# Kernel optimization log

Hardware: AMD Instinct MI355X
Metric: run time of the kernel (lower is better)

The kernel has to match this reference:

```python
import jax, jax.numpy as jnp
import numpy as np

ITEMNUM = 50000
NUM_HEADS = 4
EPS = 1e-8


def _ln(x, g, b):
    m = x.mean(-1, keepdims=True)
    v = ((x - m) ** 2).mean(-1, keepdims=True)
    return (x - m) * jax.lax.rsqrt(v + EPS) * g + b


def _forward(seqs_data, position, seqs, time_emb, pos_table, gate_W, gate_b,
             ln_attn_g, ln_attn_b, qW, qb, kW, kb, vW, vb,
             ln_ffn_g, ln_ffn_b, c1W, c1b, c2W, c2b, last_g, last_b):
    B, L, H = seqs.shape
    nb = qW.shape[0]
    hd = H // NUM_HEADS

    pe = pos_table[position]                      # [B,L,H]
    seqs = seqs + pe
    time = time_emb + pe
    # per-position per-block time gates, [B,L,nb]
    gates = jax.nn.sigmoid(jnp.einsum('blh,nh->bln', time, gate_W) + gate_b)

    keep = (seqs_data != ITEMNUM - 1)[..., None].astype(seqs.dtype)  # [B,L,1]
    seqs = seqs * keep
    tril = jnp.tril(jnp.ones((L, L), dtype=bool))  # causal: keep lower triangle
    neg_inf = jnp.asarray(-jnp.inf, seqs.dtype)
    scale = 1.0 / np.sqrt(hd).astype(np.float32)

    for i in range(nb):
        Q = _ln(seqs, ln_attn_g[i], ln_attn_b[i])
        q = Q @ qW[i].T + qb[i]
        k = time @ kW[i].T + kb[i]
        v = (seqs + time) @ vW[i].T + vb[i]
        # [B,nh,L,hd]
        q = q.reshape(B, L, NUM_HEADS, hd).transpose(0, 2, 1, 3)
        k = k.reshape(B, L, NUM_HEADS, hd).transpose(0, 2, 1, 3)
        v = v.reshape(B, L, NUM_HEADS, hd).transpose(0, 2, 1, 3)
        scores = jnp.einsum('bhqd,bhkd->bhqk', q, k) * scale  # [B,nh,L,L]
        tg = gates[:, :, i]                                   # [B,L]
        gate_mat = tg[:, None, :, None] * tg[:, None, None, :]  # [B,1,L,L] outer product
        scores = jnp.where(tril[None, None], scores * gate_mat, neg_inf)
        attn = jax.nn.softmax(scores, axis=-1)
        out = jnp.einsum('bhqk,bhkd->bhqd', attn, v)
        out = out.transpose(0, 2, 1, 3).reshape(B, L, H)
        x = Q + out
        x = _ln(x, ln_ffn_g[i], ln_ffn_b[i])
        # PointWiseFeedForward: two 1x1 convs == two linears, relu, residual
        h = jax.nn.relu(x @ c1W[i].T + c1b[i])
        seqs = (h @ c2W[i].T + c2b[i] + x) * keep

    return _ln(seqs, last_g, last_b)


def setup_inputs() -> dict:
    key = jax.random.key(0)
    B, L, H, NB, ML = 64, 512, 256, 2, 512
    ks = iter(jax.random.split(key, 32))
    nrm = lambda shape, s=0.05: jax.random.normal(next(ks), shape, jnp.float32) * s
    pos_table = nrm((ML, H), 0.02).at[0].set(0.0)  # padding_idx=0
    inp = {
        'seqs_data': jax.random.randint(next(ks), (B, L), 0, ITEMNUM - 1, jnp.int32),
        'seqs': nrm((B, L, H), 1.0),
        'position': jax.random.randint(next(ks), (B, L), 0, ML, jnp.int32),
        'time_emb': nrm((B, L, H), 1.0),
        'pos_table': pos_table,
        'gate_W': nrm((NB, H)), 'gate_b': jnp.zeros((NB,), jnp.float32),
        'ln_attn_g': jnp.ones((NB, H), jnp.float32), 'ln_attn_b': jnp.zeros((NB, H), jnp.float32),
        'qW': nrm((NB, H, H)), 'qb': jnp.zeros((NB, H), jnp.float32),
        'kW': nrm((NB, H, H)), 'kb': jnp.zeros((NB, H), jnp.float32),
        'vW': nrm((NB, H, H)), 'vb': jnp.zeros((NB, H), jnp.float32),
        'ln_ffn_g': jnp.ones((NB, H), jnp.float32), 'ln_ffn_b': jnp.zeros((NB, H), jnp.float32),
        'c1W': nrm((NB, H, H)), 'c1b': jnp.zeros((NB, H), jnp.float32),
        'c2W': nrm((NB, H, H)), 'c2b': jnp.zeros((NB, H), jnp.float32),
        'last_g': jnp.ones((H,), jnp.float32), 'last_b': jnp.zeros((H,), jnp.float32),
    }
    return inp


def reference(seqs_data, seqs, position, time_emb, pos_table, gate_W, gate_b,
              ln_attn_g, ln_attn_b, qW, qb, kW, kb, vW, vb,
              ln_ffn_g, ln_ffn_b, c1W, c1b, c2W, c2b, last_g, last_b):
    return _forward(seqs_data, position, seqs, time_emb, pos_table, gate_W, gate_b,
                    ln_attn_g, ln_attn_b, qW, qb, kW, kb, vW, vb,
                    ln_ffn_g, ln_ffn_b, c1W, c1b, c2W, c2b, last_g, last_b)
```

## Files before the change

### kernel.cpp

```cpp
#include <hip/hip_runtime.h>
#include <hip/hip_bf16.h>
#include <math.h>

#define NTOK 32768
#define Hdim 256
#define Ldim 512
#define Bdim 64
#define NHEAD 4
#define HD 64
#define PADV 49999

typedef __bf16 bf16x8 __attribute__((ext_vector_type(8)));
typedef float  f32x4  __attribute__((ext_vector_type(4)));

__device__ __forceinline__ unsigned short f2bf(float f) {
    unsigned int u = __float_as_uint(f);
    unsigned int r = (u + 0x7fffu + ((u >> 16) & 1u)) >> 16;
    return (unsigned short)r;
}
__device__ __forceinline__ float bf2f(unsigned short u) {
    return __uint_as_float(((unsigned int)u) << 16);
}

__device__ __forceinline__ void gload16(const void* g, void* l) {
    __builtin_amdgcn_global_load_lds((const __attribute__((address_space(1))) unsigned int*)g,
                                     (__attribute__((address_space(3))) unsigned int*)l,
                                     16, 0, 0);
}

__global__ __launch_bounds__(256)
void castw_kernel(const float* __restrict__ q, const float* __restrict__ k,
                  const float* __restrict__ v, const float* __restrict__ c1,
                  const float* __restrict__ c2, unsigned short* __restrict__ dst) {
    const float* srcs[5] = {q, k, v, c1, c2};
    const float* s = srcs[blockIdx.y];
    int idx = blockIdx.x * 1024 + threadIdx.x * 4;
    float4 f = *(const float4*)(s + idx);
    unsigned short* d = dst + (size_t)blockIdx.y * 131072 + idx;
    d[0] = f2bf(f.x); d[1] = f2bf(f.y); d[2] = f2bf(f.z); d[3] = f2bf(f.w);
}

__global__ __launch_bounds__(256)
void prep_ln_kernel(const int* __restrict__ seqs_data, const float* __restrict__ seqs,
                    const int* __restrict__ position, const float* __restrict__ time_emb,
                    const float* __restrict__ pos_table, const float* __restrict__ gate_W,
                    const float* __restrict__ gate_b,
                    const float* __restrict__ lnG, const float* __restrict__ lnB,
                    unsigned short* __restrict__ Tbf,
                    unsigned short* __restrict__ QXbf,
                    unsigned short* __restrict__ VINbf,
                    float* __restrict__ gates, float* __restrict__ keepv) {
    int tok  = blockIdx.x * 4 + (threadIdx.x >> 6);
    int lane = threadIdx.x & 63;
    size_t off = (size_t)tok * Hdim + lane * 4;
    int pos = position[tok];
    float4 pe = *(const float4*)(pos_table + (size_t)pos * Hdim + lane * 4);
    float4 sq = *(const float4*)(seqs + off);
    float4 tm = *(const float4*)(time_emb + off);
    float keep = (seqs_data[tok] != PADV) ? 1.0f : 0.0f;
    float4 t = {tm.x + pe.x, tm.y + pe.y, tm.z + pe.z, tm.w + pe.w};
    float4 s = {(sq.x + pe.x) * keep, (sq.y + pe.y) * keep,
                (sq.z + pe.z) * keep, (sq.w + pe.w) * keep};
    ushort4 tb = {f2bf(t.x), f2bf(t.y), f2bf(t.z), f2bf(t.w)};
    *(ushort4*)(Tbf + off) = tb;
    float4 gw0 = *(const float4*)(gate_W + lane * 4);
    float4 gw1 = *(const float4*)(gate_W + Hdim + lane * 4);
    float r0 = s.x + s.y + s.z + s.w;
    float r1 = s.x * s.x + s.y * s.y + s.z * s.z + s.w * s.w;
    float r2 = t.x * gw0.x + t.y * gw0.y + t.z * gw0.z + t.w * gw0.w;
    float r3 = t.x * gw1.x + t.y * gw1.y + t.z * gw1.z + t.w * gw1.w;
#pragma unroll
    for (int o = 1; o < 64; o <<= 1) {
        r0 += __shfl_xor(r0, o, 64);
        r1 += __shfl_xor(r1, o, 64);
        r2 += __shfl_xor(r2, o, 64);
        r3 += __shfl_xor(r3, o, 64);
    }
    float mean = r0 * (1.0f / Hdim);
    float var  = fmaxf(r1 * (1.0f / Hdim) - mean * mean, 0.0f);
    float rstd = rsqrtf(var + 1e-8f);
    if (lane == 0) {
        gates[(size_t)tok * 2 + 0] = 1.0f / (1.0f + __expf(-(r2 + gate_b[0])));
        gates[(size_t)tok * 2 + 1] = 1.0f / (1.0f + __expf(-(r3 + gate_b[1])));
        keepv[tok] = keep;
    }
    float4 g4 = *(const float4*)(lnG + lane * 4);
    float4 b4 = *(const float4*)(lnB + lane * 4);
    float4 y = {(s.x - mean) * rstd * g4.x + b4.x, (s.y - mean) * rstd * g4.y + b4.y,
                (s.z - mean) * rstd * g4.z + b4.z, (s.w - mean) * rstd * g4.w + b4.w};
    ushort4 yb = {f2bf(y.x), f2bf(y.y), f2bf(y.z), f2bf(y.w)};
    *(ushort4*)(QXbf + off) = yb;
    ushort4 vb = {f2bf(s.x + t.x), f2bf(s.y + t.y), f2bf(s.z + t.z), f2bf(s.w + t.w)};
    *(ushort4*)(VINbf + off) = vb;
}

__global__ __launch_bounds__(256)
void ln2_kernel(unsigned short* QXbf, const unsigned short* __restrict__ QA,
                const float* __restrict__ lnG, const float* __restrict__ lnB) {
    int tok  = blockIdx.x * 4 + (threadIdx.x >> 6);
    int lane = threadIdx.x & 63;
    size_t off = (size_t)tok * Hdim + lane * 4;
    ushort4 q = *(const ushort4*)(QXbf + off);
    ushort4 a = *(const ushort4*)(QA + off);
    float4 x = {bf2f(q.x) + bf2f(a.x), bf2f(q.y) + bf2f(a.y),
                bf2f(q.z) + bf2f(a.z), bf2f(q.w) + bf2f(a.w)};
    float r0 = x.x + x.y + x.z + x.w;
    float r1 = x.x * x.x + x.y * x.y + x.z * x.z + x.w * x.w;
#pragma unroll
    for (int o = 1; o < 64; o <<= 1) {
        r0 += __shfl_xor(r0, o, 64);
        r1 += __shfl_xor(r1, o, 64);
    }
    float mean = r0 * (1.0f / Hdim);
    float var  = fmaxf(r1 * (1.0f / Hdim) - mean * mean, 0.0f);
    float rstd = rsqrtf(var + 1e-8f);
    float4 g4 = *(const float4*)(lnG + lane * 4);
    float4 b4 = *(const float4*)(lnB + lane * 4);
    ushort4 yb = {f2bf((x.x - mean) * rstd * g4.x + b4.x),
                  f2bf((x.y - mean) * rstd * g4.y + b4.y),
                  f2bf((x.z - mean) * rstd * g4.z + b4.z),
                  f2bf((x.w - mean) * rstd * g4.w + b4.w)};
    *(ushort4*)(QXbf + off) = yb;
}

__global__ __launch_bounds__(256)
void lnout_kernel(const unsigned short* __restrict__ Zbf,
                  unsigned short* QXbf,
                  const unsigned short* __restrict__ Tbf,
                  const float* __restrict__ keepv,
                  const float* __restrict__ lnG, const float* __restrict__ lnB,
                  float* __restrict__ outF,
                  unsigned short* __restrict__ outVIN) {
    int tok  = blockIdx.x * 4 + (threadIdx.x >> 6);
    int lane = threadIdx.x & 63;
    size_t off = (size_t)tok * Hdim + lane * 4;
    ushort4 z = *(const ushort4*)(Zbf + off);
    ushort4 x = *(const ushort4*)(QXbf + off);
    float kf = keepv[tok];
    float4 s = {(bf2f(z.x) + bf2f(x.x)) * kf, (bf2f(z.y) + bf2f(x.y)) * kf,
                (bf2f(z.z) + bf2f(x.z)) * kf, (bf2f(z.w) + bf2f(x.w)) * kf};
    float r0 = s.x + s.y + s.z + s.w;
    float r1 = s.x * s.x + s.y * s.y + s.z * s.z + s.w * s.w;
#pragma unroll
    for (int o = 1; o < 64; o <<= 1) {
        r0 += __shfl_xor(r0, o, 64);
        r1 += __shfl_xor(r1, o, 64);
    }
    float mean = r0 * (1.0f / Hdim);
    float var  = fmaxf(r1 * (1.0f / Hdim) - mean * mean, 0.0f);
    float rstd = rsqrtf(var + 1e-8f);
    float4 g4 = *(const float4*)(lnG + lane * 4);
    float4 b4 = *(const float4*)(lnB + lane * 4);
    float4 y = {(s.x - mean) * rstd * g4.x + b4.x, (s.y - mean) * rstd * g4.y + b4.y,
                (s.z - mean) * rstd * g4.z + b4.z, (s.w - mean) * rstd * g4.w + b4.w};
    if (outF) {
        *(float4*)(outF + off) = y;
    } else {
        ushort4 yb = {f2bf(y.x), f2bf(y.y), f2bf(y.z), f2bf(y.w)};
        *(ushort4*)(QXbf + off) = yb;
        ushort4 t = *(const ushort4*)(Tbf + off);
        ushort4 vb = {f2bf(s.x + bf2f(t.x)), f2bf(s.y + bf2f(t.y)),
                      f2bf(s.z + bf2f(t.z)), f2bf(s.w + bf2f(t.w))};
        *(ushort4*)(outVIN + off) = vb;
    }
}

#define GBM 128
#define GBN 128
#define GBK 32

__global__ __launch_bounds__(256)
void gemm_qkv_kernel(const unsigned short* __restrict__ QXbf,
                     const unsigned short* __restrict__ Tbf,
                     const unsigned short* __restrict__ VINbf,
                     const unsigned short* __restrict__ qW,
                     const unsigned short* __restrict__ kW,
                     const unsigned short* __restrict__ vW,
                     const float* __restrict__ qb, const float* __restrict__ kb,
                     const float* __restrict__ vb,
                     unsigned short* __restrict__ Qbf,
                     unsigned short* __restrict__ Kbf,
                     unsigned short* __restrict__ VT) {
    __shared__ __align__(16) char smem[128 * 136 * 2];
    __bf16 (*As)[GBK] = (__bf16 (*)[GBK])smem;
    __bf16 (*Ws)[GBK] = (__bf16 (*)[GBK])(smem + 8192);
    __bf16 (*Ct)[136] = (__bf16 (*)[136])smem;
    int z = blockIdx.z;
    const unsigned short* A = (z == 0) ? QXbf : (z == 1) ? Tbf : VINbf;
    const unsigned short* W = (z == 0) ? qW : (z == 1) ? kW : vW;
    const float* bias       = (z == 0) ? qb : (z == 1) ? kb : vb;

    int tid = threadIdx.x, lane = tid & 63, w = tid >> 6;
    int wr = w >> 1, wc = w & 1;
    int m0 = blockIdx.y * GBM, n0 = blockIdx.x * GBN;
    f32x4 acc[4][4];
#pragma unroll
    for (int i = 0; i < 4; ++i)
#pragma unroll
        for (int j = 0; j < 4; ++j) acc[i][j] = (f32x4)(0.0f);
    int cA = tid, cB = tid + 256;
    int rA = cA >> 2, kA = (cA & 3) * 8;
    int rB = cB >> 2, kB = (cB & 3) * 8;
    int colq = lane & 15, kq = (lane >> 4) * 8;
    for (int kc = 0; kc < Hdim; kc += GBK) {
        __syncthreads();
        gload16(A + (size_t)(m0 + rA) * Hdim + kc + kA, (__bf16*)As + cA * 8);
        gload16(A + (size_t)(m0 + rB) * Hdim + kc + kB, (__bf16*)As + cB * 8);
        gload16(W + (size_t)(n0 + rA) * Hdim + kc + kA, (__bf16*)Ws + cA * 8);
        gload16(W + (size_t)(n0 + rB) * Hdim + kc + kB, (__bf16*)Ws + cB * 8);
        __syncthreads();
        bf16x8 af[4], bfr[4];
#pragma unroll
        for (int i = 0; i < 4; ++i)
            af[i] = *(const bf16x8*)&As[wr * 64 + i * 16 + colq][kq];
#pragma unroll
        for (int j = 0; j < 4; ++j)
            bfr[j] = *(const bf16x8*)&Ws[wc * 64 + j * 16 + colq][kq];
#pragma unroll
        for (int i = 0; i < 4; ++i)
#pragma unroll
            for (int j = 0; j < 4; ++j)
                acc[i][j] = __builtin_amdgcn_mfma_f32_16x16x32_bf16(af[i], bfr[j], acc[i][j], 0, 0, 0);
    }
    int rowq = (lane >> 4) * 4;
    if (z < 2) {
        unsigned short* outBF = (z == 0) ? Qbf : Kbf;
#pragma unroll
        for (int i = 0; i < 4; ++i)
#pragma unroll
            for (int r = 0; r < 4; ++r) {
                int m = m0 + wr * 64 + i * 16 + rowq + r;
#pragma unroll
                for (int j = 0; j < 4; ++j) {
                    int n = n0 + wc * 64 + j * 16 + colq;
                    outBF[(size_t)m * Hdim + n] = f2bf(acc[i][j][r] + bias[n]);
                }
            }
    } else {
        __syncthreads();
#pragma unroll
        for (int i = 0; i < 4; ++i)
#pragma unroll
            for (int r = 0; r < 4; ++r) {
                int ml = wr * 64 + i * 16 + rowq + r;
#pragma unroll
                for (int j = 0; j < 4; ++j) {
                    int nl = wc * 64 + j * 16 + colq;
                    Ct[nl][ml] = (__bf16)(acc[i][j][r] + bias[n0 + nl]);
                }
            }
        __syncthreads();
        int bb = m0 >> 9, l0 = m0 & 511;
#pragma unroll
        for (int it = 0; it < 8; ++it) {
            int c = tid + it * 256;
            int nl = c >> 4;
            int o8 = (c & 15) * 8;
            int n = n0 + nl;
            int hh = n >> 6, dd = n & 63;
            bf16x8 v = *(const bf16x8*)&Ct[nl][o8];
            *(bf16x8*)(VT + ((((size_t)bb * NHEAD + hh) * HD + dd) * Ldim + l0 + o8)) = v;
        }
    }
}

__global__ __launch_bounds__(256)
void gemm_plain_kernel(const unsigned short* __restrict__ A,
                       const unsigned short* __restrict__ W,
                       const float* __restrict__ bias,
                       unsigned short* __restrict__ outBF, int doRelu) {
    __shared__ __bf16 As[GBM][GBK];
    __shared__ __bf16 Ws[GBN][GBK];
    int tid = threadIdx.x, lane = tid & 63, w = tid >> 6;
    int wr = w >> 1, wc = w & 1;
    int m0 = blockIdx.y * GBM, n0 = blockIdx.x * GBN;
    f32x4 acc[4][4];
#pragma unroll
    for (int i = 0; i < 4; ++i)
#pragma unroll
        for (int j = 0; j < 4; ++j) acc[i][j] = (f32x4)(0.0f);
    int cA = tid, cB = tid + 256;
    int rA = cA >> 2, kA = (cA & 3) * 8;
    int rB = cB >> 2, kB = (cB & 3) * 8;
    int colq = lane & 15, kq = (lane >> 4) * 8;
    for (int kc = 0; kc < Hdim; kc += GBK) {
        __syncthreads();
        gload16(A + (size_t)(m0 + rA) * Hdim + kc + kA, (__bf16*)As + cA * 8);
        gload16(A + (size_t)(m0 + rB) * Hdim + kc + kB, (__bf16*)As + cB * 8);
        gload16(W + (size_t)(n0 + rA) * Hdim + kc + kA, (__bf16*)Ws + cA * 8);
        gload16(W + (size_t)(n0 + rB) * Hdim + kc + kB, (__bf16*)Ws + cB * 8);
        __syncthreads();
        bf16x8 af[4], bfr[4];
#pragma unroll
        for (int i = 0; i < 4; ++i)
            af[i] = *(const bf16x8*)&As[wr * 64 + i * 16 + colq][kq];
#pragma unroll
        for (int j = 0; j < 4; ++j)
            bfr[j] = *(const bf16x8*)&Ws[wc * 64 + j * 16 + colq][kq];
#pragma unroll
        for (int i = 0; i < 4; ++i)
#pragma unroll
            for (int j = 0; j < 4; ++j)
                acc[i][j] = __builtin_amdgcn_mfma_f32_16x16x32_bf16(af[i], bfr[j], acc[i][j], 0, 0, 0);
    }
    int rowq = (lane >> 4) * 4;
#pragma unroll
    for (int i = 0; i < 4; ++i)
#pragma unroll
        for (int r = 0; r < 4; ++r) {
            int m = m0 + wr * 64 + i * 16 + rowq + r;
#pragma unroll
            for (int j = 0; j < 4; ++j) {
                int n = n0 + wc * 64 + j * 16 + colq;
                float v = acc[i][j][r] + bias[n];
                if (doRelu) v = fmaxf(v, 0.0f);
                outBF[(size_t)m * Hdim + n] = f2bf(v);
            }
        }
}

#define AK_STRIDE 72
#define AV_STRIDE 520
#define ATTN_LDS (512 * AK_STRIDE * 2 + 64 * AV_STRIDE * 2 + 128 * AK_STRIDE * 2)
__global__ __launch_bounds__(512, 1)
void attn_mfma_kernel(const unsigned short* __restrict__ Qg,
                      const unsigned short* __restrict__ Kg,
                      const unsigned short* __restrict__ VTg,
                      const float* __restrict__ gates,
                      unsigned short* __restrict__ Ob, int blk) {
    extern __shared__ __align__(16) char smem[];
    __bf16 (*Ks)[AK_STRIDE]  = (__bf16 (*)[AK_STRIDE])smem;
    __bf16 (*VTs)[AV_STRIDE] = (__bf16 (*)[AV_STRIDE])(smem + 512 * AK_STRIDE * 2);
    __bf16 (*QPs)[AK_STRIDE] = (__bf16 (*)[AK_STRIDE])(smem + 512 * AK_STRIDE * 2 + 64 * AV_STRIDE * 2);
    int h = blockIdx.x & 3, b = blockIdx.x >> 2;
    int tid = threadIdx.x, lane = tid & 63, w = tid >> 6;
    int colq = lane & 15, grp = lane >> 4;
    int rowq = grp * 4, kq = grp * 8;

    size_t baseK = (size_t)b * Ldim * Hdim + h * HD;
#pragma unroll
    for (int it = 0; it < 8; ++it) {
        int c = tid + it * 512;
        int r = c >> 3, o = (c & 7) * 8;
        *(bf16x8*)&Ks[r][o] = *(const bf16x8*)(Kg + baseK + (size_t)r * Hdim + o);
    }
    size_t baseV = ((size_t)b * NHEAD + h) * HD * Ldim;
#pragma unroll
    for (int it = 0; it < 8; ++it) {
        int c = tid + it * 512;
        int d = c >> 6, k = (c & 63) * 8;
        *(bf16x8*)&VTs[d][k] = *(const bf16x8*)(VTg + baseV + (size_t)d * Ldim + k);
    }

    const float lscale = 0.125f * 1.44269504f;
    for (int qt = 0; qt < 4; ++qt) {
        int q0 = qt * 128;
        __syncthreads();
#pragma unroll
        for (int it = 0; it < 2; ++it) {
            int c = tid + it * 512;
            int r = c >> 3, o = (c & 7) * 8;
            *(bf16x8*)&QPs[r][o] =
                *(const bf16x8*)(Qg + (size_t)(b * Ldim + q0 + r) * Hdim + h * HD + o);
        }
        float gql[4];
#pragma unroll
        for (int r = 0; r < 4; ++r)
            gql[r] = gates[((size_t)b * Ldim + q0 + w * 16 + rowq + r) * 2 + blk] * lscale;
        __syncthreads();
        bf16x8 afq0 = *(const bf16x8*)&QPs[w * 16 + colq][kq];
        bf16x8 afq1 = *(const bf16x8*)&QPs[w * 16 + colq][32 + kq];

        float lrun[4] = {0.0f, 0.0f, 0.0f, 0.0f};
        f32x4 accO[4];
#pragma unroll
        for (int jd = 0; jd < 4; ++jd) accO[jd] = (f32x4)(0.0f);

        int nkt = 2 * qt + 2;
        for (int kt = 0; kt < nkt; ++kt) {
            int k0 = kt * 64;
            f32x4 s[4];
#pragma unroll
            for (int j = 0; j < 4; ++j) s[j] = (f32x4)(0.0f);
#pragma unroll
            for (int j = 0; j < 4; ++j) {
                bf16x8 bk0 = *(const bf16x8*)&Ks[k0 + j * 16 + colq][kq];
                bf16x8 bk1 = *(const bf16x8*)&Ks[k0 + j * 16 + colq][32 + kq];
                s[j] = __builtin_amdgcn_mfma_f32_16x16x32_bf16(afq0, bk0, s[j], 0, 0, 0);
                s[j] = __builtin_amdgcn_mfma_f32_16x16x32_bf16(afq1, bk1, s[j], 0, 0, 0);
            }
            float gkv[4];
#pragma unroll
            for (int j = 0; j < 4; ++j)
                gkv[j] = gates[((size_t)b * Ldim + k0 + j * 16 + colq) * 2 + blk];
#pragma unroll
            for (int r = 0; r < 4; ++r) {
                int qg = q0 + w * 16 + rowq + r;
                float su = 0.0f;
                float p[4];
#pragma unroll
                for (int j = 0; j < 4; ++j) {
                    int kg = k0 + j * 16 + colq;
                    float v = s[j][r] * gql[r] * gkv[j];
                    v = (kg > qg) ? -1e38f : v;
                    float e = exp2f(v);
                    p[j] = e;
                    su += e;
                }
#pragma unroll
                for (int off = 1; off < 16; off <<= 1)
                    su += __shfl_xor(su, off, 16);
                lrun[r] += su;
#pragma unroll
                for (int j = 0; j < 4; ++j)
                    QPs[w * 16 + rowq + r][j * 16 + colq] = (__bf16)p[j];
            }
            bf16x8 ap0 = *(const bf16x8*)&QPs[w * 16 + colq][kq];
            bf16x8 ap1 = *(const bf16x8*)&QPs[w * 16 + colq][32 + kq];
#pragma unroll
            for (int jd = 0; jd < 4; ++jd) {
                bf16x8 bv0 = *(const bf16x8*)&VTs[jd * 16 + colq][k0 + kq];
                bf16x8 bv1 = *(const bf16x8*)&VTs[jd * 16 + colq][k0 + 32 + kq];
                accO[jd] = __builtin_amdgcn_mfma_f32_16x16x32_bf16(ap0, bv0, accO[jd], 0, 0, 0);
                accO[jd] = __builtin_amdgcn_mfma_f32_16x16x32_bf16(ap1, bv1, accO[jd], 0, 0, 0);
            }
        }
#pragma unroll
        for (int r = 0; r < 4; ++r) {
            float inv = 1.0f / lrun[r];
#pragma unroll
            for (int jd = 0; jd < 4; ++jd)
                Ob[(size_t)(b * Ldim + q0 + w * 16 + rowq + r) * Hdim + h * HD + jd * 16 + colq] =
                    f2bf(accO[jd][r] * inv);
        }
    }
}

extern "C" void kernel_launch(void* const* d_in, const int* in_sizes, int n_in,
                              void* d_out, int out_size, void* d_ws, size_t ws_size,
                              hipStream_t stream) {
    const int*   seqs_data = (const int*)d_in[0];
    const float* seqs      = (const float*)d_in[1];
    const int*   position  = (const int*)d_in[2];
    const float* time_emb  = (const float*)d_in[3];
    const float* pos_table = (const float*)d_in[4];
    const float* gate_W    = (const float*)d_in[5];
    const float* gate_b    = (const float*)d_in[6];
    const float* ln_attn_g = (const float*)d_in[7];
    const float* ln_attn_b = (const float*)d_in[8];
    const float* qW        = (const float*)d_in[9];
    const float* qb        = (const float*)d_in[10];
    const float* kW        = (const float*)d_in[11];
    const float* kb        = (const float*)d_in[12];
    const float* vW        = (const float*)d_in[13];
    const float* vb        = (const float*)d_in[14];
    const float* ln_ffn_g  = (const float*)d_in[15];
    const float* ln_ffn_b  = (const float*)d_in[16];
    const float* c1W       = (const float*)d_in[17];
    const float* c1b       = (const float*)d_in[18];
    const float* c2W       = (const float*)d_in[19];
    const float* c2b       = (const float*)d_in[20];
    const float* last_g    = (const float*)d_in[21];
    const float* last_b    = (const float*)d_in[22];

    size_t BUF = (size_t)NTOK * Hdim;
    float* fws = (float*)d_ws;
    float* GATES = fws;
    float* KEEP  = GATES + (size_t)NTOK * 2;
    unsigned short* bws   = (unsigned short*)(KEEP + NTOK);
    unsigned short* Tbf   = bws;
    unsigned short* QXbf  = Tbf + BUF;
    unsigned short* VINbf = QXbf + BUF;
    unsigned short* HIDbf = VINbf + BUF;
    unsigned short* Qbf   = HIDbf + BUF;
    unsigned short* Kbf   = Qbf + BUF;
    unsigned short* VTbf  = Kbf + BUF;
    unsigned short* QAbf  = VTbf + BUF;
    unsigned short* Zbf   = QAbf + BUF;
    unsigned short* Wbf   = Zbf + BUF;
    size_t WB = (size_t)Hdim * Hdim;
    unsigned short* qWbf  = Wbf;
    unsigned short* kWbf  = Wbf + 2 * WB;
    unsigned short* vWbf  = Wbf + 4 * WB;
    unsigned short* c1Wbf = Wbf + 6 * WB;
    unsigned short* c2Wbf = Wbf + 8 * WB;

    castw_kernel<<<dim3(128, 5), 256, 0, stream>>>(qW, kW, vW, c1W, c2W, Wbf);
    prep_ln_kernel<<<NTOK / 4, 256, 0, stream>>>(seqs_data, seqs, position, time_emb,
                                                 pos_table, gate_W, gate_b,
                                                 ln_attn_g, ln_attn_b,
                                                 Tbf, QXbf, VINbf, GATES, KEEP);

    dim3 qkvgrid(Hdim / GBN, NTOK / GBM, 3);
    dim3 ggrid(Hdim / GBN, NTOK / GBM);
    for (int i = 0; i < 2; ++i) {
        gemm_qkv_kernel<<<qkvgrid, 256, 0, stream>>>(QXbf, Tbf, VINbf,
                                                     qWbf + i * WB, kWbf + i * WB, vWbf + i * WB,
                                                     qb + i * Hdim, kb + i * Hdim, vb + i * Hdim,
                                                     Qbf, Kbf, VTbf);
        attn_mfma_kernel<<<Bdim * NHEAD, 512, ATTN_LDS, stream>>>(Qbf, Kbf, VTbf, GATES, QAbf, i);
        ln2_kernel<<<NTOK / 4, 256, 0, stream>>>(QXbf, QAbf,
                                                 ln_ffn_g + i * Hdim, ln_ffn_b + i * Hdim);
        gemm_plain_kernel<<<ggrid, 256, 0, stream>>>(QXbf, c1Wbf + i * WB, c1b + i * Hdim, HIDbf, 1);
        gemm_plain_kernel<<<ggrid, 256, 0, stream>>>(HIDbf, c2Wbf + i * WB, c2b + i * Hdim, Zbf, 0);
        if (i == 0) {
            lnout_kernel<<<NTOK / 4, 256, 0, stream>>>(
                Zbf, QXbf, Tbf, KEEP,
                ln_attn_g + Hdim, ln_attn_b + Hdim,
                nullptr, VINbf);
        } else {
            lnout_kernel<<<NTOK / 4, 256, 0, stream>>>(
                Zbf, QXbf, Tbf, KEEP,
                last_g, last_b,
                (float*)d_out, nullptr);
        }
    }
}
```

Baseline: 390.3 us.

## Rebalance causal attention work across waves with 32-row query tiles and diagonal-only masking

Each wave now owns 32 query rows and processes two query tiles chosen in pairs (0 with 3, 1 with 2), so every wave gets a similar causal workload and the per-tile block-wide syncs go away. Q fragments are loaded straight from global memory into registers instead of being staged through LDS, and each K tile load is reused for two 16-row query subtiles. The causal mask is applied only on the diagonal key tile, and key tiles past the diagonal are skipped at 32-row granularity. The cost is more registers per wave and more serial work per wave, which may lengthen the critical path.

```diff
diff --git a/kernel.cpp b/kernel.cpp
--- a/kernel.cpp
+++ b/kernel.cpp
@@ -331,7 +331,7 @@
     extern __shared__ __align__(16) char smem[];
     __bf16 (*Ks)[AK_STRIDE]  = (__bf16 (*)[AK_STRIDE])smem;
     __bf16 (*VTs)[AV_STRIDE] = (__bf16 (*)[AV_STRIDE])(smem + 512 * AK_STRIDE * 2);
-    __bf16 (*QPs)[AK_STRIDE] = (__bf16 (*)[AK_STRIDE])(smem + 512 * AK_STRIDE * 2 + 64 * AV_STRIDE * 2);
+    __bf16 (*Ps)[AK_STRIDE]  = (__bf16 (*)[AK_STRIDE])(smem + 512 * AK_STRIDE * 2 + 64 * AV_STRIDE * 2);
     int h = blockIdx.x & 3, b = blockIdx.x >> 2;
     int tid = threadIdx.x, lane = tid & 63, w = tid >> 6;
     int colq = lane & 15, grp = lane >> 4;
@@ -351,88 +351,116 @@
         int d = c >> 6, k = (c & 63) * 8;
         *(bf16x8*)&VTs[d][k] = *(const bf16x8*)(VTg + baseV + (size_t)d * Ldim + k);
     }
+    __syncthreads();
 
     const float lscale = 0.125f * 1.44269504f;
-    for (int qt = 0; qt < 4; ++qt) {
-        int q0 = qt * 128;
-        __syncthreads();
-#pragma unroll
-        for (int it = 0; it < 2; ++it) {
-            int c = tid + it * 512;
-            int r = c >> 3, o = (c & 7) * 8;
-            *(bf16x8*)&QPs[r][o] =
-                *(const bf16x8*)(Qg + (size_t)(b * Ldim + q0 + r) * Hdim + h * HD + o);
+    int wq = w & 3;
+    int diagBand = wq >> 1;
+
+    for (int p = 0; p < 2; ++p) {
+        int qt = (w < 4) ? (p ? 3 : 0) : (p ? 2 : 1);
+        int q0 = qt * 128 + wq * 32;
+
+        bf16x8 afq[2][2];
+        float gql[2][4];
+#pragma unroll
+        for (int s = 0; s < 2; ++s) {
+            size_t qrow = (size_t)(b * Ldim + q0 + s * 16 + colq) * Hdim + h * HD;
+            afq[s][0] = *(const bf16x8*)(Qg + qrow + kq);
+            afq[s][1] = *(const bf16x8*)(Qg + qrow + 32 + kq);
+#pragma unroll
+            for (int r = 0; r < 4; ++r)
+                gql[s][r] = gates[((size_t)b * Ldim + q0 + s * 16 + rowq + r) * 2 + blk] * lscale;
         }
-        float gql[4];
-#pragma unroll
-        for (int r = 0; r < 4; ++r)
-            gql[r] = gates[((size_t)b * Ldim + q0 + w * 16 + rowq + r) * 2 + blk] * lscale;
-        __syncthreads();
-        bf16x8 afq0 = *(const bf16x8*)&QPs[w * 16 + colq][kq];
-        bf16x8 afq1 = *(const bf16x8*)&QPs[w * 16 + colq][32 + kq];
-
-        float lrun[4] = {0.0f, 0.0f, 0.0f, 0.0f};
-        f32x4 accO[4];
-#pragma unroll
-        for (int jd = 0; jd < 4; ++jd) accO[jd] = (f32x4)(0.0f);
-
-        int nkt = 2 * qt + 2;
-        for (int kt = 0; kt < nkt; ++kt) {
+
+        float lrun[2][4];
+        f32x4 accO[2][4];
+#pragma unroll
+        for (int s = 0; s < 2; ++s)
+#pragma unroll
+            for (int r = 0; r < 4; ++r) lrun[s][r] = 0.0f;
+#pragma unroll
+        for (int s = 0; s < 2; ++s)
+#pragma unroll
+            for (int jd = 0; jd < 4; ++jd) accO[s][jd] = (f32x4)(0.0f);
+
+        int nfull = qt * 2 + diagBand;
+        for (int kt = 0; kt <= nfull; ++kt) {
             int k0 = kt * 64;
-            f32x4 s[4];
-#pragma unroll
-            for (int j = 0; j < 4; ++j) s[j] = (f32x4)(0.0f);
+            bool diag = (kt == nfull);
+            f32x4 sv[2][4];
+#pragma unroll
+            for (int s = 0; s < 2; ++s)
+#pragma unroll
+                for (int j = 0; j < 4; ++j) sv[s][j] = (f32x4)(0.0f);
 #pragma unroll
             for (int j = 0; j < 4; ++j) {
                 bf16x8 bk0 = *(const bf16x8*)&Ks[k0 + j * 16 + colq][kq];
                 bf16x8 bk1 = *(const bf16x8*)&Ks[k0 + j * 16 + colq][32 + kq];
-                s[j] = __builtin_amdgcn_mfma_f32_16x16x32_bf16(afq0, bk0, s[j], 0, 0, 0);
-                s[j] = __builtin_amdgcn_mfma_f32_16x16x32_bf16(afq1, bk1, s[j], 0, 0, 0);
+#pragma unroll
+                for (int s = 0; s < 2; ++s) {
+                    sv[s][j] = __builtin_amdgcn_mfma_f32_16x16x32_bf16(afq[s][0], bk0, sv[s][j], 0, 0, 0);
+                    sv[s][j] = __builtin_amdgcn_mfma_f32_16x16x32_bf16(afq[s][1], bk1, sv[s][j], 0, 0, 0);
+                }
             }
             float gkv[4];
 #pragma unroll
             for (int j = 0; j < 4; ++j)
                 gkv[j] = gates[((size_t)b * Ldim + k0 + j * 16 + colq) * 2 + blk];
-#pragma unroll
-            for (int r = 0; r < 4; ++r) {
-                int qg = q0 + w * 16 + rowq + r;
-                float su = 0.0f;
-                float p[4];
-#pragma unroll
-                for (int j = 0; j < 4; ++j) {
-                    int kg = k0 + j * 16 + colq;
-                    float v = s[j][r] * gql[r] * gkv[j];
-                    v = (kg > qg) ? -1e38f : v;
-                    float e = exp2f(v);
-                    p[j] = e;
-                    su += e;
+
+#pragma unroll
+            for (int s = 0; s < 2; ++s) {
+#pragma unroll
+                for (int r = 0; r < 4; ++r) {
+                    float su = 0.0f;
+                    float p4[4];
+                    if (diag) {
+                        int qg = q0 + s * 16 + rowq + r;
+#pragma unroll
+                        for (int j = 0; j < 4; ++j) {
+                            float v = sv[s][j][r] * gql[s][r] * gkv[j];
+                            v = (k0 + j * 16 + colq > qg) ? -1e38f : v;
+                            float e = exp2f(v);
+                            p4[j] = e;
+                            su += e;
+                        }
+                    } else {
+#pragma unroll
+                        for (int j = 0; j < 4; ++j) {
+                            float e = exp2f(sv[s][j][r] * gql[s][r] * gkv[j]);
+                            p4[j] = e;
+                            su += e;
+                        }
+                    }
+#pragma unroll
+                    for (int off = 1; off < 16; off <<= 1)
+                        su += __shfl_xor(su, off, 16);
+                    lrun[s][r] += su;
+#pragma unroll
+                    for (int j = 0; j < 4; ++j)
+                        Ps[w * 16 + rowq + r][j * 16 + colq] = (__bf16)p4[j];
                 }
-#pragma unroll
-                for (int off = 1; off < 16; off <<= 1)
-                    su += __shfl_xor(su, off, 16);
-                lrun[r] += su;
-#pragma unroll
-                for (int j = 0; j < 4; ++j)
-                    QPs[w * 16 + rowq + r][j * 16 + colq] = (__bf16)p[j];
-            }
-            bf16x8 ap0 = *(const bf16x8*)&QPs[w * 16 + colq][kq];
-            bf16x8 ap1 = *(const bf16x8*)&QPs[w * 16 + colq][32 + kq];
-#pragma unroll
-            for (int jd = 0; jd < 4; ++jd) {
-                bf16x8 bv0 = *(const bf16x8*)&VTs[jd * 16 + colq][k0 + kq];
-                bf16x8 bv1 = *(const bf16x8*)&VTs[jd * 16 + colq][k0 + 32 + kq];
-                accO[jd] = __builtin_amdgcn_mfma_f32_16x16x32_bf16(ap0, bv0, accO[jd], 0, 0, 0);
-                accO[jd] = __builtin_amdgcn_mfma_f32_16x16x32_bf16(ap1, bv1, accO[jd], 0, 0, 0);
+                bf16x8 ap0 = *(const bf16x8*)&Ps[w * 16 + colq][kq];
+                bf16x8 ap1 = *(const bf16x8*)&Ps[w * 16 + colq][32 + kq];
+#pragma unroll
+                for (int jd = 0; jd < 4; ++jd) {
+                    bf16x8 bv0 = *(const bf16x8*)&VTs[jd * 16 + colq][k0 + kq];
+                    bf16x8 bv1 = *(const bf16x8*)&VTs[jd * 16 + colq][k0 + 32 + kq];
+                    accO[s][jd] = __builtin_amdgcn_mfma_f32_16x16x32_bf16(ap0, bv0, accO[s][jd], 0, 0, 0);
+                    accO[s][jd] = __builtin_amdgcn_mfma_f32_16x16x32_bf16(ap1, bv1, accO[s][jd], 0, 0, 0);
+                }
             }
         }
 #pragma unroll
-        for (int r = 0; r < 4; ++r) {
-            float inv = 1.0f / lrun[r];
-#pragma unroll
-            for (int jd = 0; jd < 4; ++jd)
-                Ob[(size_t)(b * Ldim + q0 + w * 16 + rowq + r) * Hdim + h * HD + jd * 16 + colq] =
-                    f2bf(accO[jd][r] * inv);
-        }
+        for (int s = 0; s < 2; ++s)
+#pragma unroll
+            for (int r = 0; r < 4; ++r) {
+                float inv = 1.0f / lrun[s][r];
+#pragma unroll
+                for (int jd = 0; jd < 4; ++jd)
+                    Ob[(size_t)(b * Ldim + q0 + s * 16 + rowq + r) * Hdim + h * HD + jd * 16 + colq] =
+                        f2bf(accO[s][jd][r] * inv);
+            }
     }
 }
 
```

After: 383.9 us. About the same (-1.6%).

## Rebalance causal attention work across 12 waves with 16-row query groups

Applied to the files above, without the earlier changes.

The attention kernel now runs 12 waves per block. Each wave owns two or three fixed 16-row query groups, chosen so that causal work is balanced across waves, and it no longer sweeps 128-row tiles with block-wide barriers. Q fragments load directly from global memory, and the per-tile barriers are gone. The causal mask is applied only on the diagonal key tile, and LDS strides are padded to 68/516 with split 8-byte accesses to cut bank conflicts. The risks are higher register pressure from 768 threads and more LDS instructions from the split loads.

```diff
diff --git a/kernel.cpp b/kernel.cpp
--- a/kernel.cpp
+++ b/kernel.cpp
@@ -11,7 +11,10 @@
 #define PADV 49999
 
 typedef __bf16 bf16x8 __attribute__((ext_vector_type(8)));
+typedef __bf16 bf16x4 __attribute__((ext_vector_type(4)));
 typedef float  f32x4  __attribute__((ext_vector_type(4)));
+
+union bf8u { bf16x8 v8; bf16x4 v4[2]; };
 
 __device__ __forceinline__ unsigned short f2bf(float f) {
     unsigned int u = __float_as_uint(f);
@@ -319,93 +322,109 @@
         }
 }
 
-#define AK_STRIDE 72
-#define AV_STRIDE 520
-#define ATTN_LDS (512 * AK_STRIDE * 2 + 64 * AV_STRIDE * 2 + 128 * AK_STRIDE * 2)
-__global__ __launch_bounds__(512, 1)
+#define AKS 68
+#define AVS 516
+#define APS 68
+#define ATTN_LDS (512 * AKS * 2 + 64 * AVS * 2 + 192 * APS * 2)
+__global__ __launch_bounds__(768, 1)
 void attn_mfma_kernel(const unsigned short* __restrict__ Qg,
                       const unsigned short* __restrict__ Kg,
                       const unsigned short* __restrict__ VTg,
                       const float* __restrict__ gates,
                       unsigned short* __restrict__ Ob, int blk) {
     extern __shared__ __align__(16) char smem[];
-    __bf16 (*Ks)[AK_STRIDE]  = (__bf16 (*)[AK_STRIDE])smem;
-    __bf16 (*VTs)[AV_STRIDE] = (__bf16 (*)[AV_STRIDE])(smem + 512 * AK_STRIDE * 2);
-    __bf16 (*QPs)[AK_STRIDE] = (__bf16 (*)[AK_STRIDE])(smem + 512 * AK_STRIDE * 2 + 64 * AV_STRIDE * 2);
+    __bf16 (*Ks)[AKS]  = (__bf16 (*)[AKS])smem;
+    __bf16 (*VTs)[AVS] = (__bf16 (*)[AVS])(smem + 512 * AKS * 2);
+    __bf16 (*Ps)[APS]  = (__bf16 (*)[APS])(smem + 512 * AKS * 2 + 64 * AVS * 2);
     int h = blockIdx.x & 3, b = blockIdx.x >> 2;
     int tid = threadIdx.x, lane = tid & 63, w = tid >> 6;
     int colq = lane & 15, grp = lane >> 4;
     int rowq = grp * 4, kq = grp * 8;
 
     size_t baseK = (size_t)b * Ldim * Hdim + h * HD;
-#pragma unroll
-    for (int it = 0; it < 8; ++it) {
-        int c = tid + it * 512;
+    for (int c = tid; c < 4096; c += 768) {
         int r = c >> 3, o = (c & 7) * 8;
-        *(bf16x8*)&Ks[r][o] = *(const bf16x8*)(Kg + baseK + (size_t)r * Hdim + o);
+        bf8u u;
+        u.v8 = *(const bf16x8*)(Kg + baseK + (size_t)r * Hdim + o);
+        *(bf16x4*)&Ks[r][o]     = u.v4[0];
+        *(bf16x4*)&Ks[r][o + 4] = u.v4[1];
     }
     size_t baseV = ((size_t)b * NHEAD + h) * HD * Ldim;
-#pragma unroll
-    for (int it = 0; it < 8; ++it) {
-        int c = tid + it * 512;
+    for (int c = tid; c < 4096; c += 768) {
         int d = c >> 6, k = (c & 63) * 8;
-        *(bf16x8*)&VTs[d][k] = *(const bf16x8*)(VTg + baseV + (size_t)d * Ldim + k);
-    }
+        bf8u u;
+        u.v8 = *(const bf16x8*)(VTg + baseV + (size_t)d * Ldim + k);
+        *(bf16x4*)&VTs[d][k]     = u.v4[0];
+        *(bf16x4*)&VTs[d][k + 4] = u.v4[1];
+    }
+    __syncthreads();
 
     const float lscale = 0.125f * 1.44269504f;
-    for (int qt = 0; qt < 4; ++qt) {
-        int q0 = qt * 128;
-        __syncthreads();
-#pragma unroll
-        for (int it = 0; it < 2; ++it) {
-            int c = tid + it * 512;
-            int r = c >> 3, o = (c & 7) * 8;
-            *(bf16x8*)&QPs[r][o] =
-                *(const bf16x8*)(Qg + (size_t)(b * Ldim + q0 + r) * Hdim + h * HD + o);
-        }
+    int gl[3], ng;
+    if (w < 4)      { gl[0] = w;     gl[1] = 8 + w;  gl[2] = 28 + w; ng = 3; }
+    else if (w < 8) { gl[0] = w;     gl[1] = 8 + w;  gl[2] = 16 + w; ng = 3; }
+    else            { gl[0] = 8 + w; gl[1] = 16 + w; gl[2] = 0;      ng = 2; }
+
+    for (int gi = 0; gi < ng; ++gi) {
+        int g = gl[gi];
+        int q0 = g * 16;
+        size_t qrow = (size_t)(b * Ldim + q0 + colq) * Hdim + h * HD;
+        bf16x8 afq0 = *(const bf16x8*)(Qg + qrow + kq);
+        bf16x8 afq1 = *(const bf16x8*)(Qg + qrow + 32 + kq);
         float gql[4];
 #pragma unroll
         for (int r = 0; r < 4; ++r)
-            gql[r] = gates[((size_t)b * Ldim + q0 + w * 16 + rowq + r) * 2 + blk] * lscale;
-        __syncthreads();
-        bf16x8 afq0 = *(const bf16x8*)&QPs[w * 16 + colq][kq];
-        bf16x8 afq1 = *(const bf16x8*)&QPs[w * 16 + colq][32 + kq];
+            gql[r] = gates[((size_t)b * Ldim + q0 + rowq + r) * 2 + blk] * lscale;
 
         float lrun[4] = {0.0f, 0.0f, 0.0f, 0.0f};
         f32x4 accO[4];
 #pragma unroll
         for (int jd = 0; jd < 4; ++jd) accO[jd] = (f32x4)(0.0f);
 
-        int nkt = 2 * qt + 2;
-        for (int kt = 0; kt < nkt; ++kt) {
+        int nfull = g >> 2;
+        for (int kt = 0; kt <= nfull; ++kt) {
             int k0 = kt * 64;
-            f32x4 s[4];
-#pragma unroll
-            for (int j = 0; j < 4; ++j) s[j] = (f32x4)(0.0f);
+            bool diag = (kt == nfull);
+            f32x4 sv[4];
+#pragma unroll
+            for (int j = 0; j < 4; ++j) sv[j] = (f32x4)(0.0f);
 #pragma unroll
             for (int j = 0; j < 4; ++j) {
-                bf16x8 bk0 = *(const bf16x8*)&Ks[k0 + j * 16 + colq][kq];
-                bf16x8 bk1 = *(const bf16x8*)&Ks[k0 + j * 16 + colq][32 + kq];
-                s[j] = __builtin_amdgcn_mfma_f32_16x16x32_bf16(afq0, bk0, s[j], 0, 0, 0);
-                s[j] = __builtin_amdgcn_mfma_f32_16x16x32_bf16(afq1, bk1, s[j], 0, 0, 0);
+                int kr = k0 + j * 16 + colq;
+                bf8u b0, b1;
+                b0.v4[0] = *(const bf16x4*)&Ks[kr][kq];
+                b0.v4[1] = *(const bf16x4*)&Ks[kr][kq + 4];
+                b1.v4[0] = *(const bf16x4*)&Ks[kr][32 + kq];
+                b1.v4[1] = *(const bf16x4*)&Ks[kr][32 + kq + 4];
+                sv[j] = __builtin_amdgcn_mfma_f32_16x16x32_bf16(afq0, b0.v8, sv[j], 0, 0, 0);
+                sv[j] = __builtin_amdgcn_mfma_f32_16x16x32_bf16(afq1, b1.v8, sv[j], 0, 0, 0);
             }
             float gkv[4];
 #pragma unroll
             for (int j = 0; j < 4; ++j)
                 gkv[j] = gates[((size_t)b * Ldim + k0 + j * 16 + colq) * 2 + blk];
+
 #pragma unroll
             for (int r = 0; r < 4; ++r) {
-                int qg = q0 + w * 16 + rowq + r;
                 float su = 0.0f;
-                float p[4];
-#pragma unroll
-                for (int j = 0; j < 4; ++j) {
-                    int kg = k0 + j * 16 + colq;
-                    float v = s[j][r] * gql[r] * gkv[j];
-                    v = (kg > qg) ? -1e38f : v;
-                    float e = exp2f(v);
-                    p[j] = e;
-                    su += e;
+                float p4[4];
+                if (diag) {
+                    int qg = q0 + rowq + r;
+#pragma unroll
+                    for (int j = 0; j < 4; ++j) {
+                        float v = sv[j][r] * gql[r] * gkv[j];
+                        v = (k0 + j * 16 + colq > qg) ? -1e38f : v;
+                        float e = exp2f(v);
+                        p4[j] = e;
+                        su += e;
+                    }
+                } else {
+#pragma unroll
+                    for (int j = 0; j < 4; ++j) {
+                        float e = exp2f(sv[j][r] * gql[r] * gkv[j]);
+                        p4[j] = e;
+                        su += e;
+                    }
                 }
 #pragma unroll
                 for (int off = 1; off < 16; off <<= 1)
@@ -413,16 +432,24 @@
                 lrun[r] += su;
 #pragma unroll
                 for (int j = 0; j < 4; ++j)
-                    QPs[w * 16 + rowq + r][j * 16 + colq] = (__bf16)p[j];
+                    Ps[w * 16 + rowq + r][j * 16 + colq] = (__bf16)p4[j];
             }
-            bf16x8 ap0 = *(const bf16x8*)&QPs[w * 16 + colq][kq];
-            bf16x8 ap1 = *(const bf16x8*)&QPs[w * 16 + colq][32 + kq];
+
+            bf8u a0, a1;
+            a0.v4[0] = *(const bf16x4*)&Ps[w * 16 + colq][kq];
+            a0.v4[1] = *(const bf16x4*)&Ps[w * 16 + colq][kq + 4];
+            a1.v4[0] = *(const bf16x4*)&Ps[w * 16 + colq][32 + kq];
+            a1.v4[1] = *(const bf16x4*)&Ps[w * 16 + colq][32 + kq + 4];
 #pragma unroll
             for (int jd = 0; jd < 4; ++jd) {
-                bf16x8 bv0 = *(const bf16x8*)&VTs[jd * 16 + colq][k0 + kq];
-                bf16x8 bv1 = *(const bf16x8*)&VTs[jd * 16 + colq][k0 + 32 + kq];
-                accO[jd] = __builtin_amdgcn_mfma_f32_16x16x32_bf16(ap0, bv0, accO[jd], 0, 0, 0);
-                accO[jd] = __builtin_amdgcn_mfma_f32_16x16x32_bf16(ap1, bv1, accO[jd], 0, 0, 0);
+                int vr = jd * 16 + colq;
+                bf8u v0, v1;
+                v0.v4[0] = *(const bf16x4*)&VTs[vr][k0 + kq];
+                v0.v4[1] = *(const bf16x4*)&VTs[vr][k0 + kq + 4];
+                v1.v4[0] = *(const bf16x4*)&VTs[vr][k0 + 32 + kq];
+                v1.v4[1] = *(const bf16x4*)&VTs[vr][k0 + 32 + kq + 4];
+                accO[jd] = __builtin_amdgcn_mfma_f32_16x16x32_bf16(a0.v8, v0.v8, accO[jd], 0, 0, 0);
+                accO[jd] = __builtin_amdgcn_mfma_f32_16x16x32_bf16(a1.v8, v1.v8, accO[jd], 0, 0, 0);
             }
         }
 #pragma unroll
@@ -430,7 +457,7 @@
             float inv = 1.0f / lrun[r];
 #pragma unroll
             for (int jd = 0; jd < 4; ++jd)
-                Ob[(size_t)(b * Ldim + q0 + w * 16 + rowq + r) * Hdim + h * HD + jd * 16 + colq] =
+                Ob[(size_t)(b * Ldim + q0 + rowq + r) * Hdim + h * HD + jd * 16 + colq] =
                     f2bf(accO[jd][r] * inv);
         }
     }
@@ -498,7 +525,7 @@
                                                      qWbf + i * WB, kWbf + i * WB, vWbf + i * WB,
                                                      qb + i * Hdim, kb + i * Hdim, vb + i * Hdim,
                                                      Qbf, Kbf, VTbf);
-        attn_mfma_kernel<<<Bdim * NHEAD, 512, ATTN_LDS, stream>>>(Qbf, Kbf, VTbf, GATES, QAbf, i);
+        attn_mfma_kernel<<<Bdim * NHEAD, 768, ATTN_LDS, stream>>>(Qbf, Kbf, VTbf, GATES, QAbf, i);
         ln2_kernel<<<NTOK / 4, 256, 0, stream>>>(QXbf, QAbf,
                                                  ln_ffn_g + i * Hdim, ln_ffn_b + i * Hdim);
         gemm_plain_kernel<<<ggrid, 256, 0, stream>>>(QXbf, c1Wbf + i * WB, c1b + i * Hdim, HIDbf, 1);
```

Result: faster. 381.2 us (-2.3%).
